# Kernel tuning notes

Hardware: AMD Instinct MI355X
Metric: run time of the kernel (lower is better)

The kernel has to match this reference:

```python
import jax, jax.numpy as jnp
import numpy as np

B, T, C, E, K = 4, 4096, 2048, 64, 8


def setup_inputs() -> dict:
    key = jax.random.key(0)
    k1, k2, k3 = jax.random.split(key, 3)
    hidden_states = jax.random.normal(k1, (B, T, C), dtype=jnp.float32)
    mask = jax.random.randint(k2, (B, T), 0, 2).astype(bool)
    gate_weight = jax.random.normal(k3, (E, C), dtype=jnp.float32) * 0.02
    gate_bias = jnp.zeros((E,), dtype=jnp.float32)
    expert_biases = jnp.zeros((E,), dtype=jnp.float32)
    return {
        "hidden_states": hidden_states,
        "mask": mask,
        "gate_weight": gate_weight,
        "gate_bias": gate_bias,
        "expert_biases": expert_biases,
    }


def reference(hidden_states, mask, gate_weight, gate_bias, expert_biases):
    Bc, Tc, Cc = hidden_states.shape
    n_experts = gate_weight.shape[0]
    x = hidden_states.reshape(-1, Cc)                 # [N, C]
    m = mask.reshape(-1)                              # [N]
    gate_output = x @ gate_weight.T + gate_bias       # [N, E]
    gate_probs = jax.nn.sigmoid(gate_output)
    gate_logits = gate_output + expert_biases
    _, top_k_indices = jax.lax.top_k(gate_logits, K)  # [N, K]
    top_k_probs = jnp.take_along_axis(gate_probs, top_k_indices, axis=-1)
    top_k_probs = top_k_probs / jnp.sum(top_k_probs, axis=-1, keepdims=True)
    # masked bincount of routed experts (only tokens where mask is True)
    weights = jnp.broadcast_to(m[:, None], top_k_indices.shape).astype(jnp.float32)
    expert_counts = jnp.zeros((n_experts,), jnp.float32).at[top_k_indices.reshape(-1)].add(weights.reshape(-1))
    avg_count = expert_counts.mean()
    maxvio = (expert_counts.max() - avg_count) / (avg_count + 1e-5)
    # note: the in-place expert_biases sign-update is a training-time, no-grad
    # side effect and does not change the returned values of this call.
    return top_k_indices, top_k_probs, maxvio
```

## Files before the change

kernel.cpp:

```cpp
#include <hip/hip_runtime.h>
#include <math.h>

#define NTOK  16384
#define CDIM  2048
#define NEXP  64
#define TOPK  8

__global__ __launch_bounds__(256) void pack_w_kernel(
    const float* __restrict__ W, float* __restrict__ Wp)
{
    int lin = blockIdx.x * 256 + threadIdx.x;
    int tx = lin & 15;
    int j  = (lin >> 4) & 3;
    int kc = (lin >> 6) & 7;
    int kt = lin >> 9;
    int e = tx * 4 + j;
    int k = kt * 32 + kc * 4;
    float4 v = *(const float4*)&W[(size_t)e * CDIM + k];
    *(float4*)&Wp[(size_t)lin * 4] = v;
}

template<int KS>
__global__ __launch_bounds__(256) void gemm_partial_kernel(
    const float* __restrict__ x,
    const float* __restrict__ Wp,
    float*       __restrict__ part)
{
    __shared__ float As[64][36];
    __shared__ float Bs[2048];

    const int tid = threadIdx.x;
    const int tx  = tid & 15;
    const int ty  = tid >> 4;
    const int bm  = blockIdx.x & 255;
    const int pp  = blockIdx.x >> 8;
    const int TILES = 64 / KS;
    const int kt0 = pp * TILES;
    const int m0  = bm * 64;

    float acc[4][4] = {};

    for (int t = 0; t < TILES; t++) {
        const int kb = (kt0 + t) * 32;
        __syncthreads();
        #pragma unroll
        for (int p = 0; p < 2; p++) {
            int lin = tid + p * 256;
            int m   = lin >> 3;
            int c4  = (lin & 7) << 2;
            *(float4*)&As[m][c4] =
                *(const float4*)&x[(size_t)(m0 + m) * CDIM + kb + c4];
        }
        const float* wsrc = Wp + (size_t)(kt0 + t) * 2048;
        #pragma unroll
        for (int p = 0; p < 2; p++) {
            int lin = tid + p * 256;
            *(float4*)&Bs[lin * 4] = *(const float4*)&wsrc[lin * 4];
        }
        __syncthreads();

        #pragma unroll
        for (int kc = 0; kc < 8; kc++) {
            float4 a[4], b[4];
            #pragma unroll
            for (int i = 0; i < 4; i++)
                a[i] = *(const float4*)&As[ty * 4 + i][kc * 4];
            #pragma unroll
            for (int j = 0; j < 4; j++)
                b[j] = *(const float4*)&Bs[((kc * 4 + j) * 16 + tx) * 4];
            #pragma unroll
            for (int i = 0; i < 4; i++)
                #pragma unroll
                for (int j = 0; j < 4; j++)
                    acc[i][j] += a[i].x * b[j].x + a[i].y * b[j].y
                               + a[i].z * b[j].z + a[i].w * b[j].w;
        }
    }

    float* dst = part + ((size_t)pp * NTOK + m0) * NEXP;
    #pragma unroll
    for (int i = 0; i < 4; i++) {
        int row = ty * 4 + i;
        float4 v = make_float4(acc[i][0], acc[i][1], acc[i][2], acc[i][3]);
        *(float4*)&dst[(size_t)row * NEXP + tx * 4] = v;
    }
}

template<int KS>
__global__ __launch_bounds__(256) void topk_kernel(
    const float* __restrict__ part,
    const int*   __restrict__ mask,
    const float* __restrict__ gbias,
    const float* __restrict__ ebias,
    float*       __restrict__ out,
    unsigned int* __restrict__ counts)
{
    __shared__ unsigned int s_cnt[NEXP];
    const int tid = threadIdx.x;
    if (tid < NEXP) s_cnt[tid] = 0u;
    __syncthreads();

    const int t = blockIdx.x * 16 + (tid >> 4);
    const int l = tid & 15;

    float4 v = make_float4(0.f, 0.f, 0.f, 0.f);
    #pragma unroll
    for (int p = 0; p < KS; p++) {
        float4 u = *(const float4*)&part[((size_t)p * NTOK + t) * NEXP + l * 4];
        v.x += u.x; v.y += u.y; v.z += u.z; v.w += u.w;
    }
    float4 gb = *(const float4*)&gbias[l * 4];
    float4 eb = *(const float4*)&ebias[l * 4];
    float z[4], sel[4];
    z[0] = v.x + gb.x; z[1] = v.y + gb.y; z[2] = v.z + gb.z; z[3] = v.w + gb.w;
    sel[0] = z[0] + eb.x; sel[1] = z[1] + eb.y;
    sel[2] = z[2] + eb.z; sel[3] = z[3] + eb.w;

    int   idxs[TOPK];
    float probs[TOPK];
    float psum = 0.f;

    #pragma unroll
    for (int r = 0; r < TOPK; r++) {
        float bv = -INFINITY; float bz = 0.f; int bidx = 1 << 30;
        #pragma unroll
        for (int i = 0; i < 4; i++) {
            if (sel[i] > bv) { bv = sel[i]; bz = z[i]; bidx = l * 4 + i; }
        }
        #pragma unroll
        for (int m = 1; m < 16; m <<= 1) {
            float ov = __shfl_xor(bv, m);
            float oz = __shfl_xor(bz, m);
            int   oi = __shfl_xor(bidx, m);
            if (ov > bv || (ov == bv && oi < bidx)) { bv = ov; bz = oz; bidx = oi; }
        }
        idxs[r] = bidx;
        float p = 1.f / (1.f + expf(-bz));
        probs[r] = p;
        psum += p;
        if ((bidx >> 2) == l) sel[bidx & 3] = -INFINITY;
    }

    float inv = 1.f / psum;
    if (l < TOPK) {
        out[(size_t)t * TOPK + l] = (float)idxs[l];
        out[(size_t)NTOK * TOPK + (size_t)t * TOPK + l] = probs[l] * inv;
        if (mask[t] != 0) atomicAdd(&s_cnt[idxs[l]], 1u);
    }
    __syncthreads();
    if (tid < NEXP && s_cnt[tid] != 0u) atomicAdd(&counts[tid], s_cnt[tid]);
}

__global__ void finalize_kernel(const unsigned int* __restrict__ counts,
                                float* __restrict__ out)
{
    const int t = threadIdx.x;
    float c  = (float)counts[t];
    float mx = c, sm = c;
    #pragma unroll
    for (int o = 32; o > 0; o >>= 1) {
        mx = fmaxf(mx, __shfl_down(mx, o));
        sm += __shfl_down(sm, o);
    }
    if (t == 0) {
        float avg = sm / (float)NEXP;
        out[2 * NTOK * TOPK] = (mx - avg) / (avg + 1e-5f);
    }
}

__global__ __launch_bounds__(256) void fused_fallback_kernel(
    const float* __restrict__ x, const int* __restrict__ mask,
    const float* __restrict__ W, const float* __restrict__ gbias,
    const float* __restrict__ ebias, float* __restrict__ out,
    unsigned int* __restrict__ counts)
{
    __shared__ float As[64][36];
    __shared__ float Bs[64][36];
    __shared__ float Lg[64][NEXP + 1];
    __shared__ float s_gb[NEXP], s_eb[NEXP];
    __shared__ unsigned int s_cnt[NEXP];

    const int tid = threadIdx.x;
    const int tx = tid & 15, ty = tid >> 4;
    const int m0 = blockIdx.x * 64;
    if (tid < NEXP) { s_gb[tid] = gbias[tid]; s_eb[tid] = ebias[tid]; s_cnt[tid] = 0u; }
    float acc[4][4] = {};
    for (int kb = 0; kb < CDIM; kb += 32) {
        __syncthreads();
        #pragma unroll
        for (int p = 0; p < 2; p++) {
            int lin = tid + p * 256; int m = lin >> 3; int c4 = (lin & 7) << 2;
            *(float4*)&As[m][c4] = *(const float4*)&x[(size_t)(m0 + m) * CDIM + kb + c4];
            *(float4*)&Bs[m][c4] = *(const float4*)&W[(size_t)m * CDIM + kb + c4];
        }
        __syncthreads();
        #pragma unroll
        for (int k4 = 0; k4 < 32; k4 += 4) {
            float4 a[4], b[4];
            #pragma unroll
            for (int i = 0; i < 4; i++) a[i] = *(const float4*)&As[ty * 4 + i][k4];
            #pragma unroll
            for (int j = 0; j < 4; j++) b[j] = *(const float4*)&Bs[tx * 4 + j][k4];
            #pragma unroll
            for (int i = 0; i < 4; i++)
                #pragma unroll
                for (int j = 0; j < 4; j++)
                    acc[i][j] += a[i].x * b[j].x + a[i].y * b[j].y
                               + a[i].z * b[j].z + a[i].w * b[j].w;
        }
    }
    __syncthreads();
    #pragma unroll
    for (int i = 0; i < 4; i++)
        #pragma unroll
        for (int j = 0; j < 4; j++)
            Lg[ty * 4 + i][tx * 4 + j] = acc[i][j] + s_gb[tx * 4 + j];
    __syncthreads();
    if (tid < 64) {
        const int g = m0 + tid;
        unsigned long long used = 0ull;
        int idxs[TOPK]; float probs[TOPK]; float psum = 0.f;
        #pragma unroll
        for (int k = 0; k < TOPK; k++) {
            float best = -INFINITY; int bi = 0;
            for (int n = 0; n < NEXP; n++) {
                if ((used >> n) & 1ull) continue;
                float vv = Lg[tid][n] + s_eb[n];
                if (vv > best) { best = vv; bi = n; }
            }
            used |= (1ull << bi);
            idxs[k] = bi;
            float p = 1.f / (1.f + expf(-Lg[tid][bi]));
            probs[k] = p; psum += p;
        }
        float inv = 1.f / psum;
        #pragma unroll
        for (int k = 0; k < TOPK; k++) {
            out[(size_t)g * TOPK + k] = (float)idxs[k];
            out[(size_t)NTOK * TOPK + (size_t)g * TOPK + k] = probs[k] * inv;
        }
        if (mask[g] != 0)
            #pragma unroll
            for (int k = 0; k < TOPK; k++) atomicAdd(&s_cnt[idxs[k]], 1u);
    }
    __syncthreads();
    if (tid < NEXP && s_cnt[tid] != 0u) atomicAdd(&counts[tid], s_cnt[tid]);
}

extern "C" void kernel_launch(void* const* d_in, const int* in_sizes, int n_in,
                              void* d_out, int out_size, void* d_ws, size_t ws_size,
                              hipStream_t stream)
{
    const float* x     = (const float*)d_in[0];
    const int*   mask  = (const int*)  d_in[1];
    const float* W     = (const float*)d_in[2];
    const float* gbias = (const float*)d_in[3];
    const float* ebias = (const float*)d_in[4];
    float* out = (float*)d_out;

    unsigned int* counts = (unsigned int*)d_ws;
    float* part = (float*)((char*)d_ws + 256);

    const size_t partB1 = (size_t)NTOK * NEXP * sizeof(float);
    const size_t wpB    = (size_t)NEXP * CDIM * sizeof(float);
    auto need = [&](int ks) { return 256 + (size_t)ks * partB1 + wpB; };

    int KS = 0;
    if      (ws_size >= need(4)) KS = 4;
    else if (ws_size >= need(2)) KS = 2;
    else if (ws_size >= need(1)) KS = 1;

    hipMemsetAsync(d_ws, 0, 256, stream);

    if (KS == 0) {
        fused_fallback_kernel<<<NTOK / 64, 256, 0, stream>>>(
            x, mask, W, gbias, ebias, out, counts);
        finalize_kernel<<<1, 64, 0, stream>>>(counts, out);
        return;
    }

    float* Wp = (float*)((char*)d_ws + 256 + (size_t)KS * partB1);
    pack_w_kernel<<<128, 256, 0, stream>>>(W, Wp);

    if (KS == 4) {
        gemm_partial_kernel<4><<<256 * 4, 256, 0, stream>>>(x, Wp, part);
        topk_kernel<4><<<NTOK / 16, 256, 0, stream>>>(part, mask, gbias, ebias, out, counts);
    } else if (KS == 2) {
        gemm_partial_kernel<2><<<256 * 2, 256, 0, stream>>>(x, Wp, part);
        topk_kernel<2><<<NTOK / 16, 256, 0, stream>>>(part, mask, gbias, ebias, out, counts);
    } else {
        gemm_partial_kernel<1><<<256 * 1, 256, 0, stream>>>(x, Wp, part);
        topk_kernel<1><<<NTOK / 16, 256, 0, stream>>>(part, mask, gbias, ebias, out, counts);
    }
    finalize_kernel<<<1, 64, 0, stream>>>(counts, out);
}
```

Measured before the change: 271.4 us.

## Add one-token-per-thread split-K gate GEMM with fused reduce and top-k

Adds a new GEMM path where each thread owns one token and keeps all 64 expert accumulators in registers. Weight values are read at wave-uniform addresses so they can be broadcast, which removes the weight-packing kernel and the LDS tiling. The reduction dimension is split 16 ways (or 8 when workspace is smaller), with partial sums stored expert-major. A new reduce kernel sums the partials through LDS and runs a per-thread top-k. The cost is per-thread strided reads of x rows, a larger partial buffer to write and read back, and high register pressure.

```diff
diff --git a/kernel.cpp b/kernel.cpp
--- a/kernel.cpp
+++ b/kernel.cpp
@@ -5,6 +5,132 @@
 #define CDIM  2048
 #define NEXP  64
 #define TOPK  8
+
+template<int KS>
+__global__ __launch_bounds__(256, 4) void gemm_rowwave_kernel(
+    const float* __restrict__ x,
+    const float* __restrict__ W,
+    float*       __restrict__ part)
+{
+    const int SL   = CDIM / KS;
+    const int tb   = blockIdx.x & 63;
+    const int pp   = blockIdx.x >> 6;
+    const int lane = threadIdx.x & 63;
+    const int wid  = threadIdx.x >> 6;
+    const int tok  = tb * 256 + wid * 64 + lane;
+    const int k0   = pp * SL;
+
+    float acc[NEXP];
+    #pragma unroll
+    for (int e = 0; e < NEXP; e++) acc[e] = 0.f;
+
+    const float* xrow = x + (size_t)tok * CDIM + k0;
+
+    for (int kc = 0; kc < SL; kc += 16) {
+        float xr[16];
+        #pragma unroll
+        for (int q = 0; q < 4; q++) {
+            float4 v = *(const float4*)&xrow[kc + q * 4];
+            xr[q*4+0] = v.x; xr[q*4+1] = v.y; xr[q*4+2] = v.z; xr[q*4+3] = v.w;
+        }
+        const float* wp = W + k0 + kc;
+        #pragma unroll
+        for (int e = 0; e < NEXP; e++) {
+            const float* we = wp + (size_t)e * CDIM;
+            #pragma unroll
+            for (int j = 0; j < 16; j++)
+                acc[e] = fmaf(xr[j], we[j], acc[e]);
+        }
+    }
+
+    float* dst = part + (size_t)pp * NEXP * NTOK + tok;
+    #pragma unroll
+    for (int e = 0; e < NEXP; e++)
+        dst[(size_t)e * NTOK] = acc[e];
+}
+
+template<int KS>
+__global__ __launch_bounds__(256) void reduce_topk_kernel(
+    const float* __restrict__ part,
+    const int*   __restrict__ mask,
+    const float* __restrict__ gbias,
+    const float* __restrict__ ebias,
+    float*       __restrict__ out,
+    unsigned int* __restrict__ counts)
+{
+    __shared__ float Ls[4][NEXP][64];
+    __shared__ unsigned int s_cnt[NEXP];
+    const int lane = threadIdx.x & 63;
+    const int wid  = threadIdx.x >> 6;
+    const int t    = blockIdx.x * 64 + lane;
+    if (threadIdx.x < NEXP) s_cnt[threadIdx.x] = 0u;
+
+    const int PPW = KS / 4;
+    float s[NEXP];
+    #pragma unroll
+    for (int e = 0; e < NEXP; e++) s[e] = 0.f;
+    for (int p = 0; p < PPW; p++) {
+        const float* src = part + (size_t)(wid * PPW + p) * NEXP * NTOK + t;
+        #pragma unroll
+        for (int e = 0; e < NEXP; e++)
+            s[e] += src[(size_t)e * NTOK];
+    }
+    #pragma unroll
+    for (int e = 0; e < NEXP; e++) Ls[wid][e][lane] = s[e];
+    __syncthreads();
+
+    if (wid == 0) {
+        float z[NEXP];
+        #pragma unroll
+        for (int e = 0; e < NEXP; e++)
+            z[e] = Ls[0][e][lane] + Ls[1][e][lane] + Ls[2][e][lane]
+                 + Ls[3][e][lane] + gbias[e];
+
+        unsigned long long used = 0ull;
+        int idxs[TOPK]; float probs[TOPK]; float psum = 0.f;
+        #pragma unroll
+        for (int r = 0; r < TOPK; r++) {
+            float bv = -INFINITY, bz = 0.f; int bi = 0;
+            #pragma unroll
+            for (int e = 0; e < NEXP; e++) {
+                float v = ((used >> e) & 1ull) ? -INFINITY : (z[e] + ebias[e]);
+                if (v > bv) { bv = v; bz = z[e]; bi = e; }
+            }
+            used |= (1ull << bi);
+            idxs[r] = bi;
+            float p = 1.f / (1.f + expf(-bz));
+            probs[r] = p; psum += p;
+        }
+        float inv = 1.f / psum;
+        #pragma unroll
+        for (int r = 0; r < TOPK; r++) {
+            out[(size_t)t * TOPK + r] = (float)idxs[r];
+            out[(size_t)NTOK * TOPK + (size_t)t * TOPK + r] = probs[r] * inv;
+        }
+        if (mask[t] != 0) {
+            #pragma unroll
+            for (int r = 0; r < TOPK; r++) atomicAdd(&s_cnt[idxs[r]], 1u);
+        }
+        atomicAdd(&counts[lane], s_cnt[lane]);
+    }
+}
+
+__global__ void finalize_kernel(const unsigned int* __restrict__ counts,
+                                float* __restrict__ out)
+{
+    const int t = threadIdx.x;
+    float c  = (float)counts[t];
+    float mx = c, sm = c;
+    #pragma unroll
+    for (int o = 32; o > 0; o >>= 1) {
+        mx = fmaxf(mx, __shfl_down(mx, o));
+        sm += __shfl_down(sm, o);
+    }
+    if (t == 0) {
+        float avg = sm / (float)NEXP;
+        out[2 * NTOK * TOPK] = (mx - avg) / (avg + 1e-5f);
+    }
+}
 
 __global__ __launch_bounds__(256) void pack_w_kernel(
     const float* __restrict__ W, float* __restrict__ Wp)
@@ -14,21 +140,17 @@
     int j  = (lin >> 4) & 3;
     int kc = (lin >> 6) & 7;
     int kt = lin >> 9;
-    int e = tx * 4 + j;
-    int k = kt * 32 + kc * 4;
-    float4 v = *(const float4*)&W[(size_t)e * CDIM + k];
+    float4 v = *(const float4*)&W[(size_t)(tx * 4 + j) * CDIM + kt * 32 + kc * 4];
     *(float4*)&Wp[(size_t)lin * 4] = v;
 }
 
 template<int KS>
 __global__ __launch_bounds__(256) void gemm_partial_kernel(
-    const float* __restrict__ x,
-    const float* __restrict__ Wp,
-    float*       __restrict__ part)
+    const float* __restrict__ x, const float* __restrict__ Wp,
+    float* __restrict__ part)
 {
     __shared__ float As[64][36];
     __shared__ float Bs[2048];
-
     const int tid = threadIdx.x;
     const int tx  = tid & 15;
     const int ty  = tid >> 4;
@@ -37,37 +159,31 @@
     const int TILES = 64 / KS;
     const int kt0 = pp * TILES;
     const int m0  = bm * 64;
-
     float acc[4][4] = {};
-
-    for (int t = 0; t < TILES; t++) {
-        const int kb = (kt0 + t) * 32;
+    for (int tt = 0; tt < TILES; tt++) {
+        const int kb = (kt0 + tt) * 32;
         __syncthreads();
         #pragma unroll
         for (int p = 0; p < 2; p++) {
             int lin = tid + p * 256;
             int m   = lin >> 3;
             int c4  = (lin & 7) << 2;
-            *(float4*)&As[m][c4] =
-                *(const float4*)&x[(size_t)(m0 + m) * CDIM + kb + c4];
-        }
-        const float* wsrc = Wp + (size_t)(kt0 + t) * 2048;
+            *(float4*)&As[m][c4] = *(const float4*)&x[(size_t)(m0 + m) * CDIM + kb + c4];
+        }
+        const float* wsrc = Wp + (size_t)(kt0 + tt) * 2048;
         #pragma unroll
         for (int p = 0; p < 2; p++) {
             int lin = tid + p * 256;
             *(float4*)&Bs[lin * 4] = *(const float4*)&wsrc[lin * 4];
         }
         __syncthreads();
-
         #pragma unroll
         for (int kc = 0; kc < 8; kc++) {
             float4 a[4], b[4];
             #pragma unroll
-            for (int i = 0; i < 4; i++)
-                a[i] = *(const float4*)&As[ty * 4 + i][kc * 4];
-            #pragma unroll
-            for (int j = 0; j < 4; j++)
-                b[j] = *(const float4*)&Bs[((kc * 4 + j) * 16 + tx) * 4];
+            for (int i = 0; i < 4; i++) a[i] = *(const float4*)&As[ty * 4 + i][kc * 4];
+            #pragma unroll
+            for (int j = 0; j < 4; j++) b[j] = *(const float4*)&Bs[((kc * 4 + j) * 16 + tx) * 4];
             #pragma unroll
             for (int i = 0; i < 4; i++)
                 #pragma unroll
@@ -76,33 +192,26 @@
                                + a[i].z * b[j].z + a[i].w * b[j].w;
         }
     }
-
     float* dst = part + ((size_t)pp * NTOK + m0) * NEXP;
     #pragma unroll
     for (int i = 0; i < 4; i++) {
-        int row = ty * 4 + i;
         float4 v = make_float4(acc[i][0], acc[i][1], acc[i][2], acc[i][3]);
-        *(float4*)&dst[(size_t)row * NEXP + tx * 4] = v;
+        *(float4*)&dst[(size_t)(ty * 4 + i) * NEXP + tx * 4] = v;
     }
 }
 
 template<int KS>
 __global__ __launch_bounds__(256) void topk_kernel(
-    const float* __restrict__ part,
-    const int*   __restrict__ mask,
-    const float* __restrict__ gbias,
-    const float* __restrict__ ebias,
-    float*       __restrict__ out,
-    unsigned int* __restrict__ counts)
+    const float* __restrict__ part, const int* __restrict__ mask,
+    const float* __restrict__ gbias, const float* __restrict__ ebias,
+    float* __restrict__ out, unsigned int* __restrict__ counts)
 {
     __shared__ unsigned int s_cnt[NEXP];
     const int tid = threadIdx.x;
     if (tid < NEXP) s_cnt[tid] = 0u;
     __syncthreads();
-
     const int t = blockIdx.x * 16 + (tid >> 4);
     const int l = tid & 15;
-
     float4 v = make_float4(0.f, 0.f, 0.f, 0.f);
     #pragma unroll
     for (int p = 0; p < KS; p++) {
@@ -113,20 +222,14 @@
     float4 eb = *(const float4*)&ebias[l * 4];
     float z[4], sel[4];
     z[0] = v.x + gb.x; z[1] = v.y + gb.y; z[2] = v.z + gb.z; z[3] = v.w + gb.w;
-    sel[0] = z[0] + eb.x; sel[1] = z[1] + eb.y;
-    sel[2] = z[2] + eb.z; sel[3] = z[3] + eb.w;
-
-    int   idxs[TOPK];
-    float probs[TOPK];
-    float psum = 0.f;
-
+    sel[0] = z[0] + eb.x; sel[1] = z[1] + eb.y; sel[2] = z[2] + eb.z; sel[3] = z[3] + eb.w;
+    int idxs[TOPK]; float probs[TOPK]; float psum = 0.f;
     #pragma unroll
     for (int r = 0; r < TOPK; r++) {
-        float bv = -INFINITY; float bz = 0.f; int bidx = 1 << 30;
-        #pragma unroll
-        for (int i = 0; i < 4; i++) {
+        float bv = -INFINITY, bz = 0.f; int bidx = 1 << 30;
+        #pragma unroll
+        for (int i = 0; i < 4; i++)
             if (sel[i] > bv) { bv = sel[i]; bz = z[i]; bidx = l * 4 + i; }
-        }
         #pragma unroll
         for (int m = 1; m < 16; m <<= 1) {
             float ov = __shfl_xor(bv, m);
@@ -136,11 +239,9 @@
         }
         idxs[r] = bidx;
         float p = 1.f / (1.f + expf(-bz));
-        probs[r] = p;
-        psum += p;
+        probs[r] = p; psum += p;
         if ((bidx >> 2) == l) sel[bidx & 3] = -INFINITY;
     }
-
     float inv = 1.f / psum;
     if (l < TOPK) {
         out[(size_t)t * TOPK + l] = (float)idxs[l];
@@ -151,23 +252,6 @@
     if (tid < NEXP && s_cnt[tid] != 0u) atomicAdd(&counts[tid], s_cnt[tid]);
 }
 
-__global__ void finalize_kernel(const unsigned int* __restrict__ counts,
-                                float* __restrict__ out)
-{
-    const int t = threadIdx.x;
-    float c  = (float)counts[t];
-    float mx = c, sm = c;
-    #pragma unroll
-    for (int o = 32; o > 0; o >>= 1) {
-        mx = fmaxf(mx, __shfl_down(mx, o));
-        sm += __shfl_down(sm, o);
-    }
-    if (t == 0) {
-        float avg = sm / (float)NEXP;
-        out[2 * NTOK * TOPK] = (mx - avg) / (avg + 1e-5f);
-    }
-}
-
 __global__ __launch_bounds__(256) void fused_fallback_kernel(
     const float* __restrict__ x, const int* __restrict__ mask,
     const float* __restrict__ W, const float* __restrict__ gbias,
@@ -179,7 +263,6 @@
     __shared__ float Lg[64][NEXP + 1];
     __shared__ float s_gb[NEXP], s_eb[NEXP];
     __shared__ unsigned int s_cnt[NEXP];
-
     const int tid = threadIdx.x;
     const int tx = tid & 15, ty = tid >> 4;
     const int m0 = blockIdx.x * 64;
@@ -263,25 +346,37 @@
 
     const size_t partB1 = (size_t)NTOK * NEXP * sizeof(float);
     const size_t wpB    = (size_t)NEXP * CDIM * sizeof(float);
-    auto need = [&](int ks) { return 256 + (size_t)ks * partB1 + wpB; };
-
-    int KS = 0;
-    if      (ws_size >= need(4)) KS = 4;
-    else if (ws_size >= need(2)) KS = 2;
-    else if (ws_size >= need(1)) KS = 1;
+    auto needC = [&](int ks) { return 256 + (size_t)ks * partB1; };
+    auto needR2 = [&](int ks) { return 256 + (size_t)ks * partB1 + wpB; };
 
     hipMemsetAsync(d_ws, 0, 256, stream);
 
-    if (KS == 0) {
-        fused_fallback_kernel<<<NTOK / 64, 256, 0, stream>>>(
-            x, mask, W, gbias, ebias, out, counts);
+    if (ws_size >= needC(16)) {
+        gemm_rowwave_kernel<16><<<64 * 16, 256, 0, stream>>>(x, W, part);
+        reduce_topk_kernel<16><<<NTOK / 64, 256, 0, stream>>>(part, mask, gbias, ebias, out, counts);
         finalize_kernel<<<1, 64, 0, stream>>>(counts, out);
         return;
     }
+    if (ws_size >= needC(8)) {
+        gemm_rowwave_kernel<8><<<64 * 8, 256, 0, stream>>>(x, W, part);
+        reduce_topk_kernel<8><<<NTOK / 64, 256, 0, stream>>>(part, mask, gbias, ebias, out, counts);
+        finalize_kernel<<<1, 64, 0, stream>>>(counts, out);
+        return;
+    }
+
+    int KS = 0;
+    if      (ws_size >= needR2(4)) KS = 4;
+    else if (ws_size >= needR2(2)) KS = 2;
+    else if (ws_size >= needR2(1)) KS = 1;
+
+    if (KS == 0) {
+        fused_fallback_kernel<<<NTOK / 64, 256, 0, stream>>>(x, mask, W, gbias, ebias, out, counts);
+        finalize_kernel<<<1, 64, 0, stream>>>(counts, out);
+        return;
+    }
 
     float* Wp = (float*)((char*)d_ws + 256 + (size_t)KS * partB1);
     pack_w_kernel<<<128, 256, 0, stream>>>(W, Wp);
-
     if (KS == 4) {
         gemm_partial_kernel<4><<<256 * 4, 256, 0, stream>>>(x, Wp, part);
         topk_kernel<4><<<NTOK / 16, 256, 0, stream>>>(part, mask, gbias, ebias, out, counts);
```

Result: slower. 472.5 us (+74.1%).
